# Optimization experiments

Measured on AMD Instinct MI355X. Metric: run time of the kernel, lower is better.

The kernel has to match this reference:

```python
import jax, jax.numpy as jnp
import numpy as np

B, C, TX, MAX_Y = 16, 192, 1024, 4096


def setup_inputs() -> dict:
    key = jax.random.key(0)
    k1, k2, k3, k4, k5 = jax.random.split(key, 5)
    return {
        "m_p": jax.random.normal(k1, (B, C, TX), dtype=jnp.float32),
        "logs_p": jax.random.normal(k2, (B, C, TX), dtype=jnp.float32),
        "logw": jax.random.normal(k3, (B, 1, TX), dtype=jnp.float32),
        "noise": jax.random.normal(k4, (B, C, MAX_Y), dtype=jnp.float32),
        "x_lengths": jax.random.randint(k5, (B,), 0, TX).astype(jnp.int32),
        "max_y": MAX_Y,
    }


def reference(m_p, logs_p, logw, noise, x_lengths, max_y):
    # m_p, logs_p: [B, C, Tx]; logw: [B, 1, Tx]; noise: [B, C, Ty]
    b, c, tx = m_p.shape
    dtype = m_p.dtype
    noise_scale = jnp.asarray(1.0, dtype)
    length_scale = jnp.asarray(1.0, dtype)

    x_len = jnp.maximum(x_lengths, 1)
    x_mask = (jnp.arange(tx)[None, :] < x_len[:, None]).astype(dtype)  # [B, Tx]

    # w = exp(logw) * x_mask * length_scale ; w_ceil = ceil(w)
    w_ceil = jnp.ceil(jnp.exp(logw[:, 0, :]) * x_mask * length_scale)  # [B, Tx]
    y_len = jnp.clip(jnp.sum(w_ceil, axis=1), 1, max_y).astype(jnp.int32)  # [B]
    y_mask = (jnp.arange(max_y)[None, :] < y_len[:, None]).astype(dtype)  # [B, Ty]

    # generate_path: monotonic alignment from cumulative durations
    cum = jnp.cumsum(w_ceil, axis=1)  # [B, Tx]
    ty = jnp.arange(max_y)
    seq = (ty[None, None, :] < cum[:, :, None]).astype(dtype)  # [B, Tx, Ty]
    path = seq - jnp.pad(seq, ((0, 0), (1, 0), (0, 0)))[:, :-1, :]  # per-token band
    attn = jnp.transpose(path, (0, 2, 1)) * x_mask[:, None, :] * y_mask[:, :, None]  # [B, Ty, Tx]

    # length regulation: expand stats to frame rate
    m_exp = jnp.einsum("byt,bct->bcy", attn, m_p)      # [B, C, Ty]
    logs_exp = jnp.einsum("byt,bct->bcy", attn, logs_p)  # [B, C, Ty]

    z_p = m_exp + noise * jnp.exp(logs_exp) * noise_scale
    return z_p, y_mask[:, None, :]
```

## Files before the change

kernel.cpp:

```cpp
#include <hip/hip_runtime.h>
#include <hip/hip_bf16.h>


__global__ void __launch_bounds__(1024) k_scan_tmap(
        const float* __restrict__ logw,
        const int* __restrict__ x_lengths,
        int* __restrict__ tmap,
        float* __restrict__ y_mask,
        int tx, int max_y) {
    const int b = blockIdx.x;
    const int t = threadIdx.x;
    __shared__ float s[1024];
    __shared__ int yl_sh;

    int xl = x_lengths[b];
    if (xl < 1) xl = 1;

    float w = 0.f;
    if (t < xl) w = ceilf(expf(logw[b * tx + t]));
    s[t] = w;
    __syncthreads();

    for (int off = 1; off < 1024; off <<= 1) {
        float v = 0.f;
        if (t >= off) v = s[t - off];
        __syncthreads();
        if (t >= off) s[t] += v;
        __syncthreads();
    }

    if (t == 0)
        yl_sh = (int)fminf(fmaxf(s[tx - 1], 1.f), (float)max_y);
    __syncthreads();
    const int yl = yl_sh;

    const int y0 = t * 4;
    int res[4];
    float msk[4];
#pragma unroll
    for (int k = 0; k < 4; ++k) {
        const int y = y0 + k;
        int r = -1;
        if (y < yl) {
            float fy = (float)y;
            int lo = 0, hi = tx - 1;
            while (lo < hi) {
                int mid = (lo + hi) >> 1;
                if (s[mid] > fy) hi = mid; else lo = mid + 1;
            }
            r = lo;
        }
        res[k] = r;
        msk[k] = (y < yl) ? 1.f : 0.f;
    }
    ((int4*)(tmap + (size_t)b * max_y))[t] =
        make_int4(res[0], res[1], res[2], res[3]);
    ((float4*)(y_mask + (size_t)b * max_y))[t] =
        make_float4(msk[0], msk[1], msk[2], msk[3]);
}

__global__ void __launch_bounds__(256) k_expand3(
        const float* __restrict__ m_p,
        const float* __restrict__ logs_p,
        const float* __restrict__ noise,
        const int* __restrict__ tmap,
        float* __restrict__ z,
        int C, int tx, int max_y) {
    __shared__ float sm[2][1024];
    __shared__ float se[2][1024];

    const int tid   = threadIdx.x;
    const int chunk = blockIdx.x;
    const int b     = chunk / (C >> 1);
    const int c0    = (chunk - b * (C >> 1)) * 2;
    const size_t row0 = (size_t)b * C + c0;

#pragma unroll
    for (int r = 0; r < 2; ++r) {
        float4 mv = ((const float4*)(m_p    + (row0 + r) * tx))[tid];
        float4 lv = ((const float4*)(logs_p + (row0 + r) * tx))[tid];
        int j = tid * 4;
        sm[r][j + 0] = mv.x; sm[r][j + 1] = mv.y;
        sm[r][j + 2] = mv.z; sm[r][j + 3] = mv.w;
        se[r][j + 0] = expf(lv.x); se[r][j + 1] = expf(lv.y);
        se[r][j + 2] = expf(lv.z); se[r][j + 3] = expf(lv.w);
    }
    __syncthreads();

    const int4* t4 = (const int4*)(tmap + (size_t)b * max_y);

    int4   tv[4];
    float4 nv[4][2];
#pragma unroll
    for (int it = 0; it < 4; ++it)
        tv[it] = t4[tid + it * 256];
#pragma unroll
    for (int it = 0; it < 4; ++it) {
        const int i = tid + it * 256;
#pragma unroll
        for (int r = 0; r < 2; ++r)
            nv[it][r] = ((const float4*)(noise + (row0 + r) * max_y))[i];
    }

#pragma unroll
    for (int it = 0; it < 4; ++it) {
        const int i = tid + it * 256;
        const int4 t = tv[it];
#pragma unroll
        for (int r = 0; r < 2; ++r) {
            const float4 n = nv[it][r];
            float4 o;
            o.x = (t.x >= 0) ? fmaf(n.x, se[r][t.x], sm[r][t.x]) : n.x;
            o.y = (t.y >= 0) ? fmaf(n.y, se[r][t.y], sm[r][t.y]) : n.y;
            o.z = (t.z >= 0) ? fmaf(n.z, se[r][t.z], sm[r][t.z]) : n.z;
            o.w = (t.w >= 0) ? fmaf(n.w, se[r][t.w], sm[r][t.w]) : n.w;
            ((float4*)(z + (row0 + r) * max_y))[i] = o;
        }
    }
}

extern "C" void kernel_launch(void* const* d_in, const int* in_sizes, int n_in,
                              void* d_out, int out_size, void* d_ws, size_t ws_size,
                              hipStream_t stream) {
    const float* m_p    = (const float*)d_in[0];
    const float* logs_p = (const float*)d_in[1];
    const float* logw   = (const float*)d_in[2];
    const float* noise  = (const float*)d_in[3];
    const int*   x_len  = (const int*)  d_in[4];

    const int B    = in_sizes[4];
    const int TX   = in_sizes[2] / B;
    const int C    = in_sizes[0] / (B * TX);
    const int MAXY = in_sizes[3] / (B * C);

    float* z      = (float*)d_out;
    float* y_mask = (float*)d_out + (size_t)B * C * MAXY;

    int* tmap = (int*)d_ws;

    k_scan_tmap<<<dim3(B), dim3(1024), 0, stream>>>(
        logw, x_len, tmap, y_mask, TX, MAXY);

    k_expand3<<<dim3(B * (C >> 1)), dim3(256), 0, stream>>>(
        m_p, logs_p, noise, tmap, z, C, TX, MAXY);
}
```

Measured before the change: 127.9 us.

## Use wave-shuffle scan, four channels per block, and nontemporal output stores

The scan kernel replaces the block-wide Hillis-Steele shared-memory scan, which needed about 20 barriers, with a wavefront shuffle scan followed by a short scan of the per-wave sums. The expand kernel now handles 4 channels per block instead of 2, so each load of the tmap row serves more channels, though each block uses more shared memory (32KB) and more noise registers. Output stores use nontemporal hints to avoid polluting the cache with streaming writes. Occupancy may drop because of the larger shared-memory and register footprint.

Result: slower. 131.6 us (+2.8%).

```diff
diff --git a/kernel.cpp b/kernel.cpp
--- a/kernel.cpp
+++ b/kernel.cpp
@@ -1,6 +1,8 @@
 #include <hip/hip_runtime.h>
 #include <hip/hip_bf16.h>
 
+
+typedef float f32x4 __attribute__((ext_vector_type(4)));
 
 __global__ void __launch_bounds__(1024) k_scan_tmap(
         const float* __restrict__ logw,
@@ -8,29 +10,43 @@
         int* __restrict__ tmap,
         float* __restrict__ y_mask,
         int tx, int max_y) {
-    const int b = blockIdx.x;
-    const int t = threadIdx.x;
+    const int b    = blockIdx.x;
+    const int t    = threadIdx.x;
+    const int lane = t & 63;
+    const int wid  = t >> 6;
     __shared__ float s[1024];
+    __shared__ float wsum[16];
     __shared__ int yl_sh;
 
     int xl = x_lengths[b];
     if (xl < 1) xl = 1;
 
-    float w = 0.f;
-    if (t < xl) w = ceilf(expf(logw[b * tx + t]));
-    s[t] = w;
+    float w = (t < xl) ? ceilf(expf(logw[b * tx + t])) : 0.f;
+
+    float v = w;
+#pragma unroll
+    for (int off = 1; off < 64; off <<= 1) {
+        float u = __shfl_up(v, off, 64);
+        if (lane >= off) v += u;
+    }
+    if (lane == 63) wsum[wid] = v;
     __syncthreads();
 
-    for (int off = 1; off < 1024; off <<= 1) {
-        float v = 0.f;
-        if (t >= off) v = s[t - off];
-        __syncthreads();
-        if (t >= off) s[t] += v;
-        __syncthreads();
+    if (wid == 0) {
+        float sv = (lane < 16) ? wsum[lane] : 0.f;
+#pragma unroll
+        for (int off = 1; off < 16; off <<= 1) {
+            float u = __shfl_up(sv, off, 64);
+            if (lane >= off) sv += u;
+        }
+        if (lane < 16) wsum[lane] = sv;
     }
+    __syncthreads();
 
-    if (t == 0)
-        yl_sh = (int)fminf(fmaxf(s[tx - 1], 1.f), (float)max_y);
+    float cum = v + ((wid > 0) ? wsum[wid - 1] : 0.f);
+    s[t] = cum;
+    if (t == tx - 1)
+        yl_sh = (int)fminf(fmaxf(cum, 1.f), (float)max_y);
     __syncthreads();
     const int yl = yl_sh;
 
@@ -59,24 +75,24 @@
         make_float4(msk[0], msk[1], msk[2], msk[3]);
 }
 
-__global__ void __launch_bounds__(256) k_expand3(
+__global__ void __launch_bounds__(256) k_expand4(
         const float* __restrict__ m_p,
         const float* __restrict__ logs_p,
         const float* __restrict__ noise,
         const int* __restrict__ tmap,
         float* __restrict__ z,
         int C, int tx, int max_y) {
-    __shared__ float sm[2][1024];
-    __shared__ float se[2][1024];
+    __shared__ float sm[4][1024];
+    __shared__ float se[4][1024];
 
-    const int tid   = threadIdx.x;
-    const int chunk = blockIdx.x;
-    const int b     = chunk / (C >> 1);
-    const int c0    = (chunk - b * (C >> 1)) * 2;
+    const int tid  = threadIdx.x;
+    const int cpB  = C >> 2;
+    const int b    = blockIdx.x / cpB;
+    const int c0   = (blockIdx.x - b * cpB) * 4;
     const size_t row0 = (size_t)b * C + c0;
 
 #pragma unroll
-    for (int r = 0; r < 2; ++r) {
+    for (int r = 0; r < 4; ++r) {
         float4 mv = ((const float4*)(m_p    + (row0 + r) * tx))[tid];
         float4 lv = ((const float4*)(logs_p + (row0 + r) * tx))[tid];
         int j = tid * 4;
@@ -90,7 +106,7 @@
     const int4* t4 = (const int4*)(tmap + (size_t)b * max_y);
 
     int4   tv[4];
-    float4 nv[4][2];
+    float4 nv[4][4];
 #pragma unroll
     for (int it = 0; it < 4; ++it)
         tv[it] = t4[tid + it * 256];
@@ -98,7 +114,7 @@
     for (int it = 0; it < 4; ++it) {
         const int i = tid + it * 256;
 #pragma unroll
-        for (int r = 0; r < 2; ++r)
+        for (int r = 0; r < 4; ++r)
             nv[it][r] = ((const float4*)(noise + (row0 + r) * max_y))[i];
     }
 
@@ -107,14 +123,15 @@
         const int i = tid + it * 256;
         const int4 t = tv[it];
 #pragma unroll
-        for (int r = 0; r < 2; ++r) {
+        for (int r = 0; r < 4; ++r) {
             const float4 n = nv[it][r];
-            float4 o;
+            f32x4 o;
             o.x = (t.x >= 0) ? fmaf(n.x, se[r][t.x], sm[r][t.x]) : n.x;
             o.y = (t.y >= 0) ? fmaf(n.y, se[r][t.y], sm[r][t.y]) : n.y;
             o.z = (t.z >= 0) ? fmaf(n.z, se[r][t.z], sm[r][t.z]) : n.z;
             o.w = (t.w >= 0) ? fmaf(n.w, se[r][t.w], sm[r][t.w]) : n.w;
-            ((float4*)(z + (row0 + r) * max_y))[i] = o;
+            __builtin_nontemporal_store(
+                o, (f32x4*)(z + (row0 + r) * max_y) + i);
         }
     }
 }
@@ -141,6 +158,6 @@
     k_scan_tmap<<<dim3(B), dim3(1024), 0, stream>>>(
         logw, x_len, tmap, y_mask, TX, MAXY);
 
-    k_expand3<<<dim3(B * (C >> 1)), dim3(256), 0, stream>>>(
+    k_expand4<<<dim3(B * (C >> 2)), dim3(256), 0, stream>>>(
         m_p, logs_p, noise, tmap, z, C, TX, MAXY);
 }
```
